# Kernel tuning notes

Measured on AMD Instinct MI355X. Metric: run time of the kernel, lower is better.

The kernel has to match this reference:

```python
import jax, jax.numpy as jnp
import numpy as np

T = 5          # temporal frames
WS = 8         # window size (square)
HEADS = 6
DIM = 192      # output channels; qkv input channels = 3*DIM
SHIFT = WS // 2
HDIM = DIM // HEADS
SCALE = HDIM ** -0.5
N = T * WS * WS  # tokens per window = 320


def _rel_index():
    # Faithful replication of the torch buffer construction (including the
    # quirk that the dw channel gets no offset).
    coords = np.stack(np.meshgrid(np.arange(T), np.arange(WS), np.arange(WS), indexing='ij'))
    cf = coords.reshape(3, -1)                      # (3, N)
    rel = (cf[:, :, None] - cf[:, None, :]).transpose(1, 2, 0).astype(np.int64)
    rel[:, :, 0] += WS - 1                          # dt channel
    rel[:, :, 1] += WS - 1                          # dh channel
    rel[:, :, 0] *= 2 * WS - 1
    return rel.sum(-1)                               # (N, N) int

REL_INDEX = jnp.asarray(_rel_index())


def setup_inputs() -> dict:
    key = jax.random.key(0)
    k1, k2, k3, k4 = jax.random.split(key, 4)
    B, H, W = 2, 64, 64
    C = 3 * DIM
    qkv = jax.random.normal(k1, (B, T * H * W, C), jnp.float32)
    bias_table = jax.random.normal(k2, ((T * 2 * WS - 1) * (2 * WS - 1), HEADS), jnp.float32) * 0.02
    proj_w = jax.random.normal(k3, (DIM, DIM), jnp.float32) / np.sqrt(DIM)
    proj_b = jax.random.normal(k4, (DIM,), jnp.float32) * 0.01
    # Standard Swin shifted-window attention mask, tiled over T (t-outer order).
    img = np.zeros((H, W), np.float32)
    cnt = 0
    sls = (slice(0, -WS), slice(-WS, -SHIFT), slice(-SHIFT, None))
    for hs in sls:
        for ws_ in sls:
            img[hs, ws_] = cnt
            cnt += 1
    mw = img.reshape(H // WS, WS, W // WS, WS).transpose(0, 2, 1, 3).reshape(-1, WS * WS)
    mw = np.tile(mw, (1, T))                         # (nW, N)
    am = mw[:, None, :] - mw[:, :, None]
    mask = jnp.asarray(np.where(am != 0, -100.0, 0.0).astype(np.float32))
    return {'qkv': qkv, 'bias_table': bias_table, 'proj_w': proj_w,
            'proj_b': proj_b, 'mask': mask, 'H': H, 'W': W}


def reference(qkv, bias_table, proj_w, proj_b, mask, H, W):
    B, L, C = qkv.shape
    x = qkv.reshape(B, T, H, W, C)
    # cyclic shift
    x = jnp.roll(x, shift=(-SHIFT, -SHIFT), axis=(2, 3))
    # window partition -> (B*nW, N, C)
    x = x.reshape(B, T, H // WS, WS, W // WS, WS, C)
    x = x.transpose(0, 2, 4, 1, 3, 5, 6).reshape(-1, N, C)
    B_ = x.shape[0]
    qkv_ = x.reshape(B_, N, 3, HEADS, HDIM).transpose(2, 0, 3, 1, 4)  # (3,B_,h,N,d)
    q, k, v = qkv_[0] * SCALE, qkv_[1], qkv_[2]
    attn = jnp.einsum('bhqd,bhkd->bhqk', q, k)       # (B_, h, N, N)
    rpb = bias_table[REL_INDEX.reshape(-1)].reshape(N, N, HEADS).transpose(2, 0, 1)
    attn = attn + rpb[None]
    nW = mask.shape[0]
    attn = attn.reshape(B_ // nW, nW, HEADS, N, N) + mask[None, :, None]
    attn = jax.nn.softmax(attn.reshape(B_, HEADS, N, N), axis=-1)
    out = jnp.einsum('bhqk,bhkd->bhqd', attn, v)     # (B_, h, N, d)
    out = out.transpose(0, 2, 1, 3).reshape(B_, N, DIM)
    out = out @ proj_w.T + proj_b
    # window reverse -> (B, T, H, W, DIM)
    out = out.reshape(B, H // WS, W // WS, T, WS, WS, DIM)
    out = out.transpose(0, 3, 1, 4, 2, 5, 6).reshape(B, T, H, W, DIM)
    out = jnp.roll(out, shift=(SHIFT, SHIFT), axis=(2, 3))
    return out.reshape(B, T * H * W, DIM)
```

## Files before the change

### kernel.cpp

```cpp
#include <hip/hip_runtime.h>
#include <hip/hip_bf16.h>

#define TT      5
#define NHEADS  6
#define DIMC    192
#define SHIFT_  4
#define HDIM_   32
#define NTOK    320
#define NWIN    64
#define BATCH   2
#define LOG2E   1.44269504088896f
#define SCALE_LOG2E (0.17677669529663687f * 1.44269504088896f)
#define NEGMASK (-100.0f * 1.44269504088896f)

typedef short short8v __attribute__((ext_vector_type(8)));
typedef float floatx4 __attribute__((ext_vector_type(4)));
union FragU { uint4 u; short8v s; };

static __device__ __forceinline__ float bf16lo(unsigned u) {
    union { unsigned i; float f; } x; x.i = u << 16; return x.f;
}
static __device__ __forceinline__ float bf16hi(unsigned u) {
    union { unsigned i; float f; } x; x.i = u & 0xffff0000u; return x.f;
}
static __device__ __forceinline__ unsigned short bf16b(float f) {
    __hip_bfloat16 h = __float2bfloat16(f);
    unsigned short u; __builtin_memcpy(&u, &h, 2); return u;
}
static __device__ __forceinline__ unsigned pk2(float a, float b) {
    return (unsigned)bf16b(a) | ((unsigned)bf16b(b) << 16);
}
static __device__ __forceinline__ unsigned pk2h(float a, float b) {
    unsigned ua = __float_as_uint(a), ub = __float_as_uint(b);
    return ((ua + 0x8000u) >> 16) | ((ub + 0x8000u) & 0xffff0000u);
}
static __device__ __forceinline__ float fexp2(float x) {
    float r;
    asm("v_exp_f32 %0, %1" : "=v"(r) : "v"(x));
    return r;
}

static __device__ __forceinline__ bool detect_bf16(const unsigned* q) {
    uint4 w = ((const uint4*)q)[threadIdx.x & 63];
    int cnt = 0;
    unsigned e;
    e = (w.x >> 7) & 0xffu; cnt += (e >= 100u && e <= 135u);
    e = (w.y >> 7) & 0xffu; cnt += (e >= 100u && e <= 135u);
    e = (w.z >> 7) & 0xffu; cnt += (e >= 100u && e <= 135u);
    e = (w.w >> 7) & 0xffu; cnt += (e >= 100u && e <= 135u);
    unsigned long long m = __ballot(cnt >= 2);
    return __popcll(m) >= 32;
}

__global__ __launch_bounds__(NTOK) void attn_mfma(
    const void* __restrict__ qkv_raw,
    const float* __restrict__ rpb,
    __hip_bfloat16* __restrict__ win_out)
{
    const bool isbf = detect_bf16((const unsigned*)qkv_raw);
    const int b_  = blockIdx.x;
    const int h   = blockIdx.y;
    const int bb  = b_ >> 6;
    const int wdx = b_ & 63;
    const int wi  = wdx >> 3, wj = wdx & 7;
    const int tid = threadIdx.x;
    const int w    = tid >> 6;
    const int lane = tid & 63;
    const int l15  = lane & 15;
    const int quad = lane >> 4;
    const int g    = lane >> 3;
    const int li   = lane & 7;

    __shared__ unsigned short sK[320 * 40];
    __shared__ unsigned short sVT[32 * 328];

    {
        const int btok = w * 64;
        if (!isbf) {
            const float* q32 = (const float*)qkv_raw;
            #pragma unroll
            for (int r = 0; r < 8; r++) {
                const int token = btok + r * 8 + g;
                const int t = token >> 6, s = token & 63;
                const int gh = (wi * 8 + (s >> 3) + SHIFT_) & 63;
                const int gw = (wj * 8 + (s & 7) + SHIFT_) & 63;
                const long grow = (long)bb * (TT * 64 * 64) + t * 4096 + gh * 64 + gw;
                const float4 kv = *(const float4*)(q32 + grow * (3 * DIMC) + DIMC + h * HDIM_ + li * 4);
                const int l32 = token & 31;
                const int slot = (token & ~31) + ((l32 & 4) << 2) + ((l32 >> 3) << 2) + (l32 & 3);
                *(uint2*)&sK[slot * 40 + li * 4] = make_uint2(pk2(kv.x, kv.y), pk2(kv.z, kv.w));
            }
            #pragma unroll
            for (int r = 0; r < 8; r++) {
                const int token = btok + r * 8 + g;
                const int t = token >> 6, s = token & 63;
                const int gh = (wi * 8 + (s >> 3) + SHIFT_) & 63;
                const int gw = (wj * 8 + (s & 7) + SHIFT_) & 63;
                const long grow = (long)bb * (TT * 64 * 64) + t * 4096 + gh * 64 + gw;
                const float4 vv = *(const float4*)(q32 + grow * (3 * DIMC) + 2 * DIMC + h * HDIM_ + li * 4);
                const int d0 = li * 4;
                sVT[(d0 + 0) * 328 + token] = bf16b(vv.x);
                sVT[(d0 + 1) * 328 + token] = bf16b(vv.y);
                sVT[(d0 + 2) * 328 + token] = bf16b(vv.z);
                sVT[(d0 + 3) * 328 + token] = bf16b(vv.w);
            }
        } else {
            const unsigned short* q16 = (const unsigned short*)qkv_raw;
            #pragma unroll
            for (int r = 0; r < 8; r++) {
                const int token = btok + r * 8 + g;
                const int t = token >> 6, s = token & 63;
                const int gh = (wi * 8 + (s >> 3) + SHIFT_) & 63;
                const int gw = (wj * 8 + (s & 7) + SHIFT_) & 63;
                const long grow = (long)bb * (TT * 64 * 64) + t * 4096 + gh * 64 + gw;
                const uint2 kv = *(const uint2*)(q16 + grow * (3 * DIMC) + DIMC + h * HDIM_ + li * 4);
                const int l32 = token & 31;
                const int slot = (token & ~31) + ((l32 & 4) << 2) + ((l32 >> 3) << 2) + (l32 & 3);
                *(uint2*)&sK[slot * 40 + li * 4] = kv;
            }
            #pragma unroll
            for (int r = 0; r < 8; r++) {
                const int token = btok + r * 8 + g;
                const int t = token >> 6, s = token & 63;
                const int gh = (wi * 8 + (s >> 3) + SHIFT_) & 63;
                const int gw = (wj * 8 + (s & 7) + SHIFT_) & 63;
                const long grow = (long)bb * (TT * 64 * 64) + t * 4096 + gh * 64 + gw;
                const uint2 vv = *(const uint2*)(q16 + grow * (3 * DIMC) + 2 * DIMC + h * HDIM_ + li * 4);
                const int d0 = li * 4;
                sVT[(d0 + 0) * 328 + token] = (unsigned short)(vv.x & 0xffffu);
                sVT[(d0 + 1) * 328 + token] = (unsigned short)(vv.x >> 16);
                sVT[(d0 + 2) * 328 + token] = (unsigned short)(vv.y & 0xffffu);
                sVT[(d0 + 3) * 328 + token] = (unsigned short)(vv.y >> 16);
            }
        }
    }

    FragU qf[4];
    int labq[4];
    const float* rq[4];
    #pragma unroll
    for (int jq = 0; jq < 4; jq++) {
        const int qtok = w * 64 + jq * 16 + l15;
        const int t = qtok >> 6, s = qtok & 63, hl = s >> 3, wl = s & 7;
        rq[jq] = rpb + ((h * NTOK + qtok) * NTOK);
        const int hh = wi * 8 + hl, ww = wj * 8 + wl;
        labq[jq] = ((hh < 56) ? 0 : ((hh < 60) ? 1 : 2)) * 3 +
                   ((ww < 56) ? 0 : ((ww < 60) ? 1 : 2));
        const int gh = (wi * 8 + hl + SHIFT_) & 63;
        const int gw = (wj * 8 + wl + SHIFT_) & 63;
        const long grow = (long)bb * (TT * 64 * 64) + t * 4096 + gh * 64 + gw;
        if (!isbf) {
            const float* qp = (const float*)qkv_raw + grow * (3 * DIMC) + h * HDIM_ + quad * 8;
            qf[jq].u = make_uint4(
                pk2(qp[0]*SCALE_LOG2E, qp[1]*SCALE_LOG2E), pk2(qp[2]*SCALE_LOG2E, qp[3]*SCALE_LOG2E),
                pk2(qp[4]*SCALE_LOG2E, qp[5]*SCALE_LOG2E), pk2(qp[6]*SCALE_LOG2E, qp[7]*SCALE_LOG2E));
        } else {
            const uint4 uu = *(const uint4*)((const __hip_bfloat16*)qkv_raw + grow * (3 * DIMC) + h * HDIM_ + quad * 8);
            qf[jq].u = make_uint4(
                pk2(bf16lo(uu.x)*SCALE_LOG2E, bf16hi(uu.x)*SCALE_LOG2E),
                pk2(bf16lo(uu.y)*SCALE_LOG2E, bf16hi(uu.y)*SCALE_LOG2E),
                pk2(bf16lo(uu.z)*SCALE_LOG2E, bf16hi(uu.z)*SCALE_LOG2E),
                pk2(bf16lo(uu.w)*SCALE_LOG2E, bf16hi(uu.w)*SCALE_LOG2E));
        }
    }
    __syncthreads();

    const floatx4 z4 = {0.f, 0.f, 0.f, 0.f};
    floatx4 oacc[4][2];
    #pragma unroll
    for (int i = 0; i < 4; i++) { oacc[i][0] = z4; oacc[i][1] = z4; }
    float rs[4] = {0.f, 0.f, 0.f, 0.f};

    for (int kb = 0; kb < 10; kb++) {
        FragU kf0, kf1, vf0, vf1;
        kf0.u = *(const uint4*)&sK[(kb * 32 + l15) * 40 + quad * 8];
        kf1.u = *(const uint4*)&sK[(kb * 32 + 16 + l15) * 40 + quad * 8];
        vf0.u = *(const uint4*)&sVT[l15 * 328 + kb * 32 + quad * 8];
        vf1.u = *(const uint4*)&sVT[(16 + l15) * 328 + kb * 32 + quad * 8];

        float4 rb0[4], rb1[4];
        #pragma unroll
        for (int jq = 0; jq < 4; jq++) {
            const float* rp = rq[jq] + kb * 32 + quad * 8;
            rb0[jq] = *(const float4*)rp;
            rb1[jq] = *(const float4*)(rp + 4);
        }

        floatx4 sv0[4], sv1[4];
        #pragma unroll
        for (int jq = 0; jq < 4; jq++)
            sv0[jq] = __builtin_amdgcn_mfma_f32_16x16x32_bf16(kf0.s, qf[jq].s, z4, 0, 0, 0);
        #pragma unroll
        for (int jq = 0; jq < 4; jq++)
            sv1[jq] = __builtin_amdgcn_mfma_f32_16x16x32_bf16(kf1.s, qf[jq].s, z4, 0, 0, 0);

        const int sh   = (kb & 1) * 4 + quad;
        const int rhk  = (wi == 7) ? ((sh < 4) ? 1 : 2) : 0;
        const int lab0 = rhk * 3 + ((wj == 7) ? 1 : 0);
        const int lab1 = rhk * 3 + ((wj == 7) ? 2 : 0);

        #pragma unroll
        for (int jq = 0; jq < 4; jq++) {
            const float m0 = (lab0 != labq[jq]) ? NEGMASK : 0.f;
            const float m1 = (lab1 != labq[jq]) ? NEGMASK : 0.f;
            float e0[4], e1[4];
            e0[0] = fexp2(sv0[jq][0] + rb0[jq].x + m0);
            e0[1] = fexp2(sv0[jq][1] + rb0[jq].y + m0);
            e0[2] = fexp2(sv0[jq][2] + rb0[jq].z + m0);
            e0[3] = fexp2(sv0[jq][3] + rb0[jq].w + m0);
            e1[0] = fexp2(sv1[jq][0] + rb1[jq].x + m1);
            e1[1] = fexp2(sv1[jq][1] + rb1[jq].y + m1);
            e1[2] = fexp2(sv1[jq][2] + rb1[jq].z + m1);
            e1[3] = fexp2(sv1[jq][3] + rb1[jq].w + m1);
            rs[jq] += ((e0[0] + e0[1]) + (e0[2] + e0[3]))
                    + ((e1[0] + e1[1]) + (e1[2] + e1[3]));
            FragU pf;
            pf.u.x = pk2h(e0[0], e0[1]); pf.u.y = pk2h(e0[2], e0[3]);
            pf.u.z = pk2h(e1[0], e1[1]); pf.u.w = pk2h(e1[2], e1[3]);
            oacc[jq][0] = __builtin_amdgcn_mfma_f32_16x16x32_bf16(vf0.s, pf.s, oacc[jq][0], 0, 0, 0);
            oacc[jq][1] = __builtin_amdgcn_mfma_f32_16x16x32_bf16(vf1.s, pf.s, oacc[jq][1], 0, 0, 0);
        }
    }

    unsigned short* wp = (unsigned short*)win_out;
    #pragma unroll
    for (int jq = 0; jq < 4; jq++) {
        float r = rs[jq];
        r += __shfl_xor(r, 16);
        r += __shfl_xor(r, 32);
        const float inv = 1.0f / r;
        const long ob = ((long)b_ * NTOK + (w * 64 + jq * 16 + l15)) * DIMC + h * HDIM_ + quad * 4;
        #pragma unroll
        for (int nt = 0; nt < 2; nt++) {
            const floatx4 o = oacc[jq][nt];
            *(uint2*)&wp[ob + nt * 16] =
                make_uint2(pk2(o[0] * inv, o[1] * inv), pk2(o[2] * inv, o[3] * inv));
        }
    }
}

__global__ __launch_bounds__(256) void prep_all(
    const void* __restrict__ w_raw, const void* __restrict__ b_raw,
    const void* __restrict__ bias_raw,
    const unsigned* __restrict__ sniff,
    unsigned short* __restrict__ wbf, float* __restrict__ bf32,
    float* __restrict__ rpb)
{
    const bool isbf = detect_bf16(sniff);
    const int g = blockIdx.x * 256 + threadIdx.x;
    if (g < 36864) {
        if (!isbf) wbf[g] = bf16b(((const float*)w_raw)[g]);
        else       wbf[g] = ((const unsigned short*)w_raw)[g];
    }
    if (g < 192) {
        bf32[g] = isbf
            ? __bfloat162float(((const __hip_bfloat16*)b_raw)[g])
            : ((const float*)b_raw)[g];
    }
    const int h = g / (NTOK * NTOK);
    const int r = g - h * (NTOK * NTOK);
    const int q = r / NTOK;
    const int k = r - q * NTOK;
    const int cnq = (q >> 6) * 15 + ((q >> 3) & 7) + (q & 7);
    const int cnk = (k >> 6) * 15 + ((k >> 3) & 7) + (k & 7);
    const int idx = (cnq - cnk + 112) * NHEADS + h;
    const float v = isbf
        ? __bfloat162float(((const __hip_bfloat16*)bias_raw)[idx])
        : ((const float*)bias_raw)[idx];
    rpb[g] = v * LOG2E;
}

__global__ __launch_bounds__(256) void proj_mfma(
    const __hip_bfloat16* __restrict__ win,
    const unsigned short* __restrict__ wbf,
    const float* __restrict__ bf32,
    const unsigned* __restrict__ sniff,
    void* __restrict__ out_raw)
{
    const bool isbf = detect_bf16(sniff);
    const int tid  = threadIdx.x;
    const int w    = tid >> 6;
    const int lane = tid & 63;
    const int l15  = lane & 15;
    const int quad = lane >> 4;
    const int tok0 = blockIdx.x * 64 + w * 16;

    __shared__ unsigned short sX[64 * 200];

    {
        const unsigned short* src = (const unsigned short*)win
                                  + (long)blockIdx.x * 64 * DIMC;
        #pragma unroll
        for (int it = 0; it < 6; it++) {
            const int j   = it * 256 + tid;
            const int tok = j / 24;
            const int d8  = j - tok * 24;
            const uint4 v = *(const uint4*)(src + j * 8);
            *(uint4*)&sX[tok * 200 + d8 * 8] = v;
        }
    }
    __syncthreads();

    const floatx4 z4 = {0.f, 0.f, 0.f, 0.f};
    floatx4 acc[12];
    #pragma unroll
    for (int nt = 0; nt < 12; nt++) acc[nt] = z4;

    #pragma unroll
    for (int ks = 0; ks < 6; ks++) {
        FragU xf;
        xf.u = *(const uint4*)&sX[(w * 16 + l15) * 200 + ks * 32 + quad * 8];
        #pragma unroll
        for (int nt = 0; nt < 12; nt++) {
            FragU wf;
            wf.u = *(const uint4*)(wbf + (nt * 16 + l15) * DIMC + ks * 32 + quad * 8);
            acc[nt] = __builtin_amdgcn_mfma_f32_16x16x32_bf16(wf.s, xf.s, acc[nt], 0, 0, 0);
        }
    }

    const int token = tok0 + l15;
    const int bw = token / NTOK;
    const int nn = token - bw * NTOK;
    const int bb = bw >> 6, wdx = bw & 63, wi2 = wdx >> 3, wj2 = wdx & 7;
    const int t = nn >> 6, s2 = nn & 63, hl = s2 >> 3, wl = s2 & 7;
    const int gh = (wi2 * 8 + hl + SHIFT_) & 63;
    const int gw = (wj2 * 8 + wl + SHIFT_) & 63;
    const long rowoff = ((long)bb * (TT * 64 * 64) + t * 4096 + gh * 64 + gw) * DIMC;

    #pragma unroll
    for (int nt = 0; nt < 12; nt++) {
        const float4 bv = *(const float4*)&bf32[nt * 16 + quad * 4];
        const float o0 = acc[nt][0] + bv.x, o1 = acc[nt][1] + bv.y;
        const float o2 = acc[nt][2] + bv.z, o3 = acc[nt][3] + bv.w;
        const long off = rowoff + nt * 16 + quad * 4;
        if (!isbf) {
            *(float4*)((float*)out_raw + off) = make_float4(o0, o1, o2, o3);
        } else {
            *(uint2*)((unsigned short*)out_raw + off) = make_uint2(pk2(o0, o1), pk2(o2, o3));
        }
    }
}

extern "C" void kernel_launch(void* const* d_in, const int* in_sizes, int n_in,
                              void* d_out, int out_size, void* d_ws, size_t ws_size,
                              hipStream_t stream)
{
    (void)in_sizes; (void)n_in; (void)out_size; (void)ws_size;
    const void* qkv        = d_in[0];
    const void* bias_table = d_in[1];
    const void* proj_w     = d_in[2];
    const void* proj_b     = d_in[3];

    __hip_bfloat16* win = (__hip_bfloat16*)d_ws;
    unsigned short* wbf = (unsigned short*)((char*)d_ws + 15728640);
    float*          bfb = (float*)((char*)d_ws + 15802368);
    float*          rpb = (float*)((char*)d_ws + 15803136);

    prep_all<<<dim3(2400), 256, 0, stream>>>(proj_w, proj_b, bias_table,
                                             (const unsigned*)qkv, wbf, bfb, rpb);
    attn_mfma<<<dim3(BATCH * NWIN, NHEADS), NTOK, 0, stream>>>(qkv, rpb, win);
    proj_mfma<<<dim3(BATCH * NWIN * NTOK / 64), 256, 0, stream>>>(
        win, wbf, bfb, (const unsigned*)qkv, d_out);
}
```

Measured before the change: 249.1 us.

## Load K fragments directly from global memory and linearize attention grid

Result: slower. 262.8 us (+5.5%).

```diff
diff --git a/kernel.cpp b/kernel.cpp
--- a/kernel.cpp
+++ b/kernel.cpp
@@ -58,8 +58,9 @@
     __hip_bfloat16* __restrict__ win_out)
 {
     const bool isbf = detect_bf16((const unsigned*)qkv_raw);
-    const int b_  = blockIdx.x;
-    const int h   = blockIdx.y;
+    const int bid = blockIdx.x;
+    const int b_  = bid / NHEADS;
+    const int h   = bid - b_ * NHEADS;
     const int bb  = b_ >> 6;
     const int wdx = b_ & 63;
     const int wi  = wdx >> 3, wj = wdx & 7;
@@ -71,25 +72,12 @@
     const int g    = lane >> 3;
     const int li   = lane & 7;
 
-    __shared__ unsigned short sK[320 * 40];
     __shared__ unsigned short sVT[32 * 328];
 
     {
         const int btok = w * 64;
         if (!isbf) {
             const float* q32 = (const float*)qkv_raw;
-            #pragma unroll
-            for (int r = 0; r < 8; r++) {
-                const int token = btok + r * 8 + g;
-                const int t = token >> 6, s = token & 63;
-                const int gh = (wi * 8 + (s >> 3) + SHIFT_) & 63;
-                const int gw = (wj * 8 + (s & 7) + SHIFT_) & 63;
-                const long grow = (long)bb * (TT * 64 * 64) + t * 4096 + gh * 64 + gw;
-                const float4 kv = *(const float4*)(q32 + grow * (3 * DIMC) + DIMC + h * HDIM_ + li * 4);
-                const int l32 = token & 31;
-                const int slot = (token & ~31) + ((l32 & 4) << 2) + ((l32 >> 3) << 2) + (l32 & 3);
-                *(uint2*)&sK[slot * 40 + li * 4] = make_uint2(pk2(kv.x, kv.y), pk2(kv.z, kv.w));
-            }
             #pragma unroll
             for (int r = 0; r < 8; r++) {
                 const int token = btok + r * 8 + g;
@@ -113,18 +101,6 @@
                 const int gh = (wi * 8 + (s >> 3) + SHIFT_) & 63;
                 const int gw = (wj * 8 + (s & 7) + SHIFT_) & 63;
                 const long grow = (long)bb * (TT * 64 * 64) + t * 4096 + gh * 64 + gw;
-                const uint2 kv = *(const uint2*)(q16 + grow * (3 * DIMC) + DIMC + h * HDIM_ + li * 4);
-                const int l32 = token & 31;
-                const int slot = (token & ~31) + ((l32 & 4) << 2) + ((l32 >> 3) << 2) + (l32 & 3);
-                *(uint2*)&sK[slot * 40 + li * 4] = kv;
-            }
-            #pragma unroll
-            for (int r = 0; r < 8; r++) {
-                const int token = btok + r * 8 + g;
-                const int t = token >> 6, s = token & 63;
-                const int gh = (wi * 8 + (s >> 3) + SHIFT_) & 63;
-                const int gw = (wj * 8 + (s & 7) + SHIFT_) & 63;
-                const long grow = (long)bb * (TT * 64 * 64) + t * 4096 + gh * 64 + gw;
                 const uint2 vv = *(const uint2*)(q16 + grow * (3 * DIMC) + 2 * DIMC + h * HDIM_ + li * 4);
                 const int d0 = li * 4;
                 sVT[(d0 + 0) * 328 + token] = (unsigned short)(vv.x & 0xffffu);
@@ -165,6 +141,8 @@
     }
     __syncthreads();
 
+    const int koff0 = ((l15 >> 2) << 3) + (l15 & 3);
+
     const floatx4 z4 = {0.f, 0.f, 0.f, 0.f};
     floatx4 oacc[4][2];
     #pragma unroll
@@ -172,9 +150,32 @@
     float rs[4] = {0.f, 0.f, 0.f, 0.f};
 
     for (int kb = 0; kb < 10; kb++) {
-        FragU kf0, kf1, vf0, vf1;
-        kf0.u = *(const uint4*)&sK[(kb * 32 + l15) * 40 + quad * 8];
-        kf1.u = *(const uint4*)&sK[(kb * 32 + 16 + l15) * 40 + quad * 8];
+        FragU kf0, kf1;
+        {
+            const int tok0 = kb * 32 + koff0;
+            const int t0 = tok0 >> 6, s0 = tok0 & 63;
+            const int gh0 = (wi * 8 + (s0 >> 3) + SHIFT_) & 63;
+            const int gw0 = (wj * 8 + (s0 & 7) + SHIFT_) & 63;
+            const long grow0 = (long)bb * (TT * 64 * 64) + t0 * 4096 + gh0 * 64 + gw0;
+            const int tok1 = tok0 + 4;
+            const int t1 = tok1 >> 6, s1 = tok1 & 63;
+            const int gh1 = (wi * 8 + (s1 >> 3) + SHIFT_) & 63;
+            const int gw1 = (wj * 8 + (s1 & 7) + SHIFT_) & 63;
+            const long grow1 = (long)bb * (TT * 64 * 64) + t1 * 4096 + gh1 * 64 + gw1;
+            if (!isbf) {
+                const float* kp0 = (const float*)qkv_raw + grow0 * (3 * DIMC) + DIMC + h * HDIM_ + quad * 8;
+                const float* kp1 = (const float*)qkv_raw + grow1 * (3 * DIMC) + DIMC + h * HDIM_ + quad * 8;
+                const float4 a0 = *(const float4*)kp0, b0 = *(const float4*)(kp0 + 4);
+                const float4 a1 = *(const float4*)kp1, b1 = *(const float4*)(kp1 + 4);
+                kf0.u = make_uint4(pk2(a0.x, a0.y), pk2(a0.z, a0.w), pk2(b0.x, b0.y), pk2(b0.z, b0.w));
+                kf1.u = make_uint4(pk2(a1.x, a1.y), pk2(a1.z, a1.w), pk2(b1.x, b1.y), pk2(b1.z, b1.w));
+            } else {
+                kf0.u = *(const uint4*)((const __hip_bfloat16*)qkv_raw + grow0 * (3 * DIMC) + DIMC + h * HDIM_ + quad * 8);
+                kf1.u = *(const uint4*)((const __hip_bfloat16*)qkv_raw + grow1 * (3 * DIMC) + DIMC + h * HDIM_ + quad * 8);
+            }
+        }
+
+        FragU vf0, vf1;
         vf0.u = *(const uint4*)&sVT[l15 * 328 + kb * 32 + quad * 8];
         vf1.u = *(const uint4*)&sVT[(16 + l15) * 328 + kb * 32 + quad * 8];
 
@@ -358,7 +359,7 @@
 
     prep_all<<<dim3(2400), 256, 0, stream>>>(proj_w, proj_b, bias_table,
                                              (const unsigned*)qkv, wbf, bfb, rpb);
-    attn_mfma<<<dim3(BATCH * NWIN, NHEADS), NTOK, 0, stream>>>(qkv, rpb, win);
+    attn_mfma<<<dim3(BATCH * NWIN * NHEADS), NTOK, 0, stream>>>(qkv, rpb, win);
     proj_mfma<<<dim3(BATCH * NWIN * NTOK / 64), 256, 0, stream>>>(
         win, wbf, bfb, (const unsigned*)qkv, d_out);
 }
```
